# Kernel tuning notes

Measured on AMD Instinct MI355X. Metric: run time of the kernel, lower is better.

## Reference

```python
import jax, jax.numpy as jnp
import numpy as np

N = 10000      # nodes
E = 50000      # edges
NS = 48        # multiplicity of 0e (scalars)
NV = 10        # multiplicity of 1o (vectors)
NEF = 128      # n_edge_features
HID = 128      # hidden_features
W1N = NS * NS  # path 0e x 0e -> 0e
W2N = NS * NV  # path 0e x 1o -> 1o
W3N = NV * NV  # path 1o x 0e -> 1o
W4N = NV * NS  # path 1o x 1o -> 0e
WTOT = W1N + W2N + W3N + W4N  # tp.weight_numel = 3364
EPS = 1e-5
INV_SQRT3 = float(1.0 / np.sqrt(3.0))   # w3j(1,1,0) coefficient
NORM0 = float(1.0 / np.sqrt(NS + NV))   # path normalization into 0e output
NORM1 = float(1.0 / np.sqrt(NS + NV))   # path normalization into 1o output


def setup_inputs() -> dict:
    key = jax.random.key(0)
    ks = jax.random.split(key, 6)
    node_attr = jax.random.normal(ks[0], (N, NS + 3 * NV), jnp.float32)
    edge_index = jax.random.randint(ks[1], (2, E), 0, N, dtype=jnp.int32)
    edge_attr = jax.random.normal(ks[2], (E, NEF), jnp.float32)
    edge_sh = jax.random.normal(ks[3], (E, 4), jnp.float32)
    fc_w1 = jax.random.normal(ks[4], (NEF, HID), jnp.float32) / np.sqrt(NEF)
    fc_b1 = jnp.zeros((HID,), jnp.float32)
    fc_w2 = jax.random.normal(ks[5], (HID, WTOT), jnp.float32) / np.sqrt(HID)
    fc_b2 = jnp.zeros((WTOT,), jnp.float32)
    bn_weight = jnp.ones((NS + NV,), jnp.float32)  # affine scale per irrep
    bn_bias = jnp.zeros((NS,), jnp.float32)        # bias only for scalars
    return {"node_attr": node_attr, "edge_index": edge_index,
            "edge_attr": edge_attr, "edge_sh": edge_sh,
            "fc_w1": fc_w1, "fc_b1": fc_b1, "fc_w2": fc_w2, "fc_b2": fc_b2,
            "bn_weight": bn_weight, "bn_bias": bn_bias}


def reference(node_attr, edge_index, edge_attr, edge_sh,
              fc_w1, fc_b1, fc_w2, fc_b2, bn_weight, bn_bias):
    edge_src, edge_dst = edge_index[0], edge_index[1]

    # gather node features per edge
    x = node_attr[edge_dst]                       # [E, 78]
    s_in = x[:, :NS]                              # [E, NS] scalars (0e)
    v_in = x[:, NS:].reshape(E, NV, 3)            # [E, NV, 3] vectors (1o)
    sh0 = edge_sh[:, 0:1]                         # [E, 1]   sh 0e
    sh1 = edge_sh[:, 1:4]                         # [E, 3]   sh 1o

    # weight-generating MLP (per-edge tensor-product weights)
    h = jax.nn.relu(edge_attr @ fc_w1 + fc_b1)
    w = h @ fc_w2 + fc_b2                         # [E, 3364]
    w1 = w[:, :W1N].reshape(E, NS, NS)
    w2 = w[:, W1N:W1N + W2N].reshape(E, NS, NV)
    w3 = w[:, W1N + W2N:W1N + W2N + W3N].reshape(E, NV, NV)
    w4 = w[:, W1N + W2N + W3N:].reshape(E, NV, NS)

    # Clebsch-Gordan tensor product (4 paths)
    dot = jnp.einsum('evi,ei->ev', v_in, sh1) * INV_SQRT3      # 1o x 1o -> 0e
    out0 = (jnp.einsum('euv,eu->ev', w1, s_in) * sh0
            + jnp.einsum('euv,eu->ev', w4, dot)) * NORM0        # [E, NS]
    out1 = (jnp.einsum('euv,eu->ev', w2, s_in)[:, :, None] * sh1[:, None, :]
            + jnp.einsum('euv,eui->evi', w3, v_in) * sh0[:, :, None]) * NORM1  # [E, NV, 3]
    tp = jnp.concatenate([out0, out1.reshape(E, 3 * NV)], axis=-1)  # [E, 78]

    # scatter-mean to nodes
    summed = jax.ops.segment_sum(tp, edge_src, num_segments=N)
    cnt = jax.ops.segment_sum(jnp.ones((E,), tp.dtype), edge_src, num_segments=N)
    out = summed / jnp.maximum(cnt, 1.0)[:, None]

    # residual (in/out dims equal, so F.pad is a no-op)
    out = out + node_attr

    # e3nn-style equivariant BatchNorm (training mode, component normalization)
    s = out[:, :NS]
    v = out[:, NS:].reshape(N, NV, 3)
    s = s - s.mean(axis=0)
    s = s * jax.lax.rsqrt((s ** 2).mean(axis=0) + EPS) * bn_weight[:NS] + bn_bias
    vn = (v ** 2).mean(axis=-1).mean(axis=0)       # [NV] mean squared component
    v = v * (jax.lax.rsqrt(vn + EPS) * bn_weight[NS:])[None, :, None]
    return jnp.concatenate([s, v.reshape(N, 3 * NV)], axis=-1)
```

## Files before the change

### kernel.cpp

```cpp
#include <hip/hip_runtime.h>
#include <hip/hip_bf16.h>

#define NS 48
#define NV 10
#define NATT 78
#define HID 128
#define WTOT 3364
#define NEDGE 50000
#define NNODE 10000
#define EPAD 50048
#define EPSV 1e-5f
#define INV_SQRT3 0.57735026918962576f
#define NORM0 0.13130643285972254f
#define NORM1 0.13130643285972254f

#define FXS  2147483648.0f
#define FXSI (1.0 / 2147483648.0)
#define FXQ  268435456.0f
#define FXQI (1.0 / 268435456.0)

#define CPAD2 3744
#define NTILE 232
#define NGRP  78

#define NBLK_NODE 256

#define PREP_BLKS 1872
#define FC1_BLKS  782
#define ZERO_BYTES 6280000
#define ZERO_BLKS 1534

#define TP_BLKS 391

using half8 = __attribute__((ext_vector_type(8))) _Float16;
using f32x4 = __attribute__((ext_vector_type(4))) float;

__device__ __forceinline__ unsigned short f2h(float x) {
  union { _Float16 h; unsigned short u; } v;
  v.h = (_Float16)x;
  return v.u;
}

__device__ __forceinline__ void atomFx(unsigned long long* p, float x) {
  long long q = (long long)rintf(x * FXS);
  atomicAdd(p, (unsigned long long)q);
}

__device__ __forceinline__ int cp_to_src(int cp) {
  if (cp < 2304) return cp;
  if (cp < 2784) return 2884 + (cp - 2304);
  if (cp < 3552) { int t = cp - 2784; int u = t >> 4, v = t & 15;
                   return (v < 10) ? (2304 + u * 10 + v) : -1; }
  if (cp < 3712) { int t = cp - 3552; int u = t >> 4, v = t & 15;
                   return (v < 10) ? (2784 + u * 10 + v) : -1; }
  return -1;
}

__global__ __launch_bounds__(256) void k_front(const float* __restrict__ w2,
                                               unsigned short* __restrict__ Bt2,
                                               const float* __restrict__ ea,
                                               const float* __restrict__ w1,
                                               const float* __restrict__ b1,
                                               unsigned short* __restrict__ hbf,
                                               char* __restrict__ zbase) {
  __shared__ _Float16 w1T[128][136];
  const int bid = blockIdx.x;
  const int tid = threadIdx.x;

  if (bid < PREP_BLKS) {
    int idx = bid * 256 + tid;
    int cp = idx >> 7, k = idx & 127;
    int c_src = cp_to_src(cp);
    Bt2[idx] = (c_src >= 0) ? f2h(w2[(size_t)k * WTOT + c_src]) : (unsigned short)0;
    return;
  }
  if (bid >= PREP_BLKS + FC1_BLKS) {
    size_t off = ((size_t)(bid - PREP_BLKS - FC1_BLKS) * 256 + tid) * 16;
    if (off < ZERO_BYTES) *(uint4*)(zbase + off) = make_uint4(0, 0, 0, 0);
    return;
  }

  const int b  = bid - PREP_BLKS;
  const int e0 = b * 64;
  for (int i = tid; i < 128 * 128; i += 256) {
    int k = i >> 7, n = i & 127;
    w1T[n][k] = (_Float16)w1[i];
  }
  __syncthreads();

  const int lane = tid & 63, wid = tid >> 6;
  const int col = lane & 15, quad = lane >> 4;
  int e  = e0 + wid * 16 + col;
  int er = (e < NEDGE) ? e : 0;
  const float* ear = ea + (size_t)er * 128;
  half8 aF[4];
  #pragma unroll
  for (int ks = 0; ks < 4; ++ks) {
    float4 x0 = *(const float4*)&ear[ks * 32 + quad * 8];
    float4 x1 = *(const float4*)&ear[ks * 32 + quad * 8 + 4];
    half8 a;
    a[0] = (_Float16)x0.x; a[1] = (_Float16)x0.y; a[2] = (_Float16)x0.z; a[3] = (_Float16)x0.w;
    a[4] = (_Float16)x1.x; a[5] = (_Float16)x1.y; a[6] = (_Float16)x1.z; a[7] = (_Float16)x1.w;
    aF[ks] = a;
  }
  const int erow = e0 + wid * 16 + quad * 4;
  #pragma unroll
  for (int t = 0; t < 8; ++t) {
    float b1c = b1[t * 16 + col];
    f32x4 m = {0.f, 0.f, 0.f, 0.f};
    #pragma unroll
    for (int ks = 0; ks < 4; ++ks) {
      half8 bf = *(const half8*)&w1T[t * 16 + col][ks * 32 + quad * 8];
      m = __builtin_amdgcn_mfma_f32_16x16x32_f16(aF[ks], bf, m, 0, 0, 0);
    }
    #pragma unroll
    for (int r = 0; r < 4; ++r) {
      float h = fmaxf(m[r] + b1c, 0.f);
      hbf[(size_t)(erow + r) * 128 + t * 16 + col] = f2h(h);
    }
  }
}

__global__ __launch_bounds__(512, 4) void k_tp(const unsigned short* __restrict__ hbf,
                                               const unsigned short* __restrict__ Bt2,
                                               const float* __restrict__ fb2,
                                               const int* __restrict__ eidx,
                                               const float* __restrict__ node_attr,
                                               const float* __restrict__ esh,
                                               unsigned long long* __restrict__ summed,
                                               unsigned* __restrict__ cnt) {
  __shared__ half8    bufB[1536];
  __shared__ _Float16 sFT[48][128];
  __shared__ _Float16 vFL[128][30];
  __shared__ _Float16 b2pH[CPAD2];

  const int tid  = threadIdx.x;
  const int wid  = tid >> 6;
  const int lane = tid & 63;
  const int col  = lane & 15;
  const int quad = lane >> 4;
  const int e0   = blockIdx.x * 128;
  const int elb  = wid * 16 + quad * 4;

  float p0v[4];
  float sh1n[4][3];
  int   srcR[4];
  #pragma unroll
  for (int r = 0; r < 4; ++r) {
    int eg = e0 + elb + r;
    bool val = eg < NEDGE;
    srcR[r] = val ? eidx[eg] : -1;
    float sh0 = 0.f, x = 0.f, y = 0.f, z = 0.f;
    if (val) {
      float4 s4 = *(const float4*)&esh[(size_t)eg * 4];
      sh0 = s4.x; x = s4.y; y = s4.z; z = s4.w;
    }
    p0v[r] = sh0 * NORM0;
    sh1n[r][0] = x * NORM1; sh1n[r][1] = y * NORM1; sh1n[r][2] = z * NORM1;
  }
  for (int i = tid; i < CPAD2; i += 512) {
    int c_src = cp_to_src(i);
    b2pH[i] = (c_src >= 0) ? (_Float16)fb2[c_src] : (_Float16)0.f;
  }
  for (int i = tid; i < 128 * NATT; i += 512) {
    int el = i / NATT, a = i % NATT;
    int eg = e0 + el;
    int dst = (eg < NEDGE) ? eidx[NEDGE + eg] : -1;
    float x = (dst >= 0) ? node_attr[(size_t)dst * NATT + a] : 0.f;
    if (a < NS) sFT[a][el] = (_Float16)x; else vFL[el][a - NS] = (_Float16)x;
  }
  __syncthreads();

  half8 aF0, aF1, aF2, aF3;
  {
    const half8* hp = (const half8*)hbf;
    size_t arow = (size_t)(e0 + wid * 16 + col) * 16;
    aF0 = hp[arow + 0 * 4 + quad];
    aF1 = hp[arow + 1 * 4 + quad];
    aF2 = hp[arow + 2 * 4 + quad];
    aF3 = hp[arow + 3 * 4 + quad];
  }

  const char* bt2c = (const char*)Bt2;
  const int colS = (tid >> 4) & 15, k8sS = tid & 15;
  const size_t gOff = (size_t)(colS * 16 + (k8sS ^ colS)) * 16;

  #define STAGE3(G) do {                                                           \
    if (wid < 4) {                                                                 \
      int _t0 = (G) * 3;                                                           \
      char* _db = (char*)bufB + ((G) & 1) * 12288 + wid * 1024;                    \
      _Pragma("unroll")                                                            \
      for (int _t = 0; _t < 3; ++_t)                                               \
        __builtin_amdgcn_global_load_lds(                                          \
          (const __attribute__((address_space(1))) void*)(bt2c + (size_t)(_t0 + _t) * 4096 + gOff), \
          (__attribute__((address_space(3))) void*)(_db + _t * 4096), 16, 0, 0);   \
    }                                                                              \
  } while (0)

  STAGE3(0); STAGE3(1);

  float acc0[4][3] = {};
  float t1a[4] = {};
  float t3a[4][3] = {};

  const int k0 = (0 * 4 + quad) ^ col;
  const int k1 = (1 * 4 + quad) ^ col;
  const int k2 = (2 * 4 + quad) ^ col;
  const int k3 = (3 * 4 + quad) ^ col;
  const int cb = col * 16;

  #pragma unroll 1
  for (int p = 0; p < NGRP; ++p) {
    asm volatile("s_waitcnt vmcnt(0)\n\ts_barrier" ::: "memory");

    const int bb = ((p & 1) << 9) + ((p & 1) << 8) + cb;
    half8 b00 = bufB[bb +   0 + k0], b01 = bufB[bb +   0 + k1],
          b02 = bufB[bb +   0 + k2], b03 = bufB[bb +   0 + k3];
    half8 b10 = bufB[bb + 256 + k0], b11 = bufB[bb + 256 + k1],
          b12 = bufB[bb + 256 + k2], b13 = bufB[bb + 256 + k3];
    half8 b20 = bufB[bb + 512 + k0], b21 = bufB[bb + 512 + k1],
          b22 = bufB[bb + 512 + k2], b23 = bufB[bb + 512 + k3];

    __builtin_amdgcn_s_setprio(1);
    f32x4 m0 = {0.f, 0.f, 0.f, 0.f};
    f32x4 m1 = {0.f, 0.f, 0.f, 0.f};
    f32x4 m2 = {0.f, 0.f, 0.f, 0.f};
    m0 = __builtin_amdgcn_mfma_f32_16x16x32_f16(aF0, b00, m0, 0, 0, 0);
    m1 = __builtin_amdgcn_mfma_f32_16x16x32_f16(aF0, b10, m1, 0, 0, 0);
    m2 = __builtin_amdgcn_mfma_f32_16x16x32_f16(aF0, b20, m2, 0, 0, 0);
    m0 = __builtin_amdgcn_mfma_f32_16x16x32_f16(aF1, b01, m0, 0, 0, 0);
    m1 = __builtin_amdgcn_mfma_f32_16x16x32_f16(aF1, b11, m1, 0, 0, 0);
    m2 = __builtin_amdgcn_mfma_f32_16x16x32_f16(aF1, b21, m2, 0, 0, 0);
    m0 = __builtin_amdgcn_mfma_f32_16x16x32_f16(aF2, b02, m0, 0, 0, 0);
    m1 = __builtin_amdgcn_mfma_f32_16x16x32_f16(aF2, b12, m1, 0, 0, 0);
    m2 = __builtin_amdgcn_mfma_f32_16x16x32_f16(aF2, b22, m2, 0, 0, 0);
    m0 = __builtin_amdgcn_mfma_f32_16x16x32_f16(aF3, b03, m0, 0, 0, 0);
    m1 = __builtin_amdgcn_mfma_f32_16x16x32_f16(aF3, b13, m1, 0, 0, 0);
    m2 = __builtin_amdgcn_mfma_f32_16x16x32_f16(aF3, b23, m2, 0, 0, 0);
    __builtin_amdgcn_s_setprio(0);

    asm volatile("s_waitcnt lgkmcnt(0)\n\ts_barrier" ::: "memory");
    if (p < NGRP - 2) STAGE3(p + 2);

    float b2c0 = (float)b2pH[(p * 3 + 0) * 16 + col];
    float b2c1 = (float)b2pH[(p * 3 + 1) * 16 + col];
    float b2c2 = (float)b2pH[(p * 3 + 2) * 16 + col];
    if (p < 48) {
      #pragma unroll
      for (int r = 0; r < 4; ++r) {
        float sfac = (float)sFT[p][elb + r] * p0v[r];
        acc0[r][0] += (m0[r] + b2c0) * sfac;
        acc0[r][1] += (m1[r] + b2c1) * sfac;
        acc0[r][2] += (m2[r] + b2c2) * sfac;
      }
    } else if (p < 58) {
      int u3 = (p - 48) * 3;
      #pragma unroll
      for (int r = 0; r < 4; ++r) {
        int el = elb + r;
        float dfac = ((float)vFL[el][u3]     * sh1n[r][0] +
                      (float)vFL[el][u3 + 1] * sh1n[r][1] +
                      (float)vFL[el][u3 + 2] * sh1n[r][2]) * INV_SQRT3;
        acc0[r][0] += (m0[r] + b2c0) * dfac;
        acc0[r][1] += (m1[r] + b2c1) * dfac;
        acc0[r][2] += (m2[r] + b2c2) * dfac;
      }
    } else if (p < 74) {
      int u0 = (p - 58) * 3;
      #pragma unroll
      for (int r = 0; r < 4; ++r) {
        int el = elb + r;
        t1a[r] += (m0[r] + b2c0) * (float)sFT[u0][el]
                + (m1[r] + b2c1) * (float)sFT[u0 + 1][el]
                + (m2[r] + b2c2) * (float)sFT[u0 + 2][el];
      }
    } else {
      int ub = (p - 74) * 3;
      int T0 = p * 3;
      #pragma unroll
      for (int r = 0; r < 4; ++r) {
        int el = elb + r;
        {
          float w = m0[r] + b2c0;
          t3a[r][0] += w * (float)vFL[el][(ub + 0) * 3 + 0];
          t3a[r][1] += w * (float)vFL[el][(ub + 0) * 3 + 1];
          t3a[r][2] += w * (float)vFL[el][(ub + 0) * 3 + 2];
        }
        if (T0 + 1 < NTILE) {
          float w = m1[r] + b2c1;
          t3a[r][0] += w * (float)vFL[el][(ub + 1) * 3 + 0];
          t3a[r][1] += w * (float)vFL[el][(ub + 1) * 3 + 1];
          t3a[r][2] += w * (float)vFL[el][(ub + 1) * 3 + 2];
        }
        if (T0 + 2 < NTILE) {
          float w = m2[r] + b2c2;
          t3a[r][0] += w * (float)vFL[el][(ub + 2) * 3 + 0];
          t3a[r][1] += w * (float)vFL[el][(ub + 2) * 3 + 1];
          t3a[r][2] += w * (float)vFL[el][(ub + 2) * 3 + 2];
        }
      }
    }
  }
  #undef STAGE3

  #pragma unroll
  for (int r = 0; r < 4; ++r) {
    int src = srcR[r];
    if (src < 0) continue;
    unsigned long long* dp = &summed[(size_t)src * NATT];
    #pragma unroll
    for (int j = 0; j < 3; ++j)
      atomFx(dp + j * 16 + col, acc0[r][j]);
    if (col < 10) {
      float q0 = p0v[r];
      #pragma unroll
      for (int i = 0; i < 3; ++i)
        atomFx(dp + NS + col * 3 + i,
               t1a[r] * sh1n[r][i] + t3a[r][i] * q0);
    }
  }
  if (tid < 128) {
    int eg = e0 + tid;
    if (eg < NEDGE) atomicAdd(&cnt[eidx[eg]], 1u);
  }
}

__global__ __launch_bounds__(256) void k_node(const unsigned long long* __restrict__ summed,
                                              const unsigned* __restrict__ cnt,
                                              const float* __restrict__ node_attr,
                                              float* __restrict__ outp,
                                              unsigned long long* __restrict__ partials) {
  __shared__ unsigned long long ls[NS], lq[NS], lv[NV];
  int tid = threadIdx.x;
  if (tid < NS) { ls[tid] = 0ull; lq[tid] = 0ull; }
  if (tid < NV) lv[tid] = 0ull;
  __syncthreads();
  for (int i = blockIdx.x * 256 + tid; i < NNODE * NATT; i += NBLK_NODE * 256) {
    int row = i / NATT, colc = i % NATT;
    long long sv = (long long)summed[i];
    float sum = (float)((double)sv * FXSI);
    float x = sum / fmaxf((float)cnt[row], 1.f) + node_attr[i];
    outp[i] = x;
    if (colc < NS) {
      atomicAdd(&ls[colc], (unsigned long long)(long long)rintf(x * FXS));
      atomicAdd(&lq[colc], (unsigned long long)(long long)rintf(x * x * FXQ));
    } else {
      atomicAdd(&lv[(colc - NS) / 3], (unsigned long long)(long long)rintf(x * x * FXQ));
    }
  }
  __syncthreads();
  if (tid < 128) {
    unsigned long long v = 0ull;
    if (tid < NS)            v = ls[tid];
    else if (tid < 2 * NS)   v = lq[tid - NS];
    else if (tid < 96 + NV)  v = lv[tid - 96];
    partials[(size_t)blockIdx.x * 128 + tid] = v;
  }
}

__global__ __launch_bounds__(128) void k_stats(const unsigned long long* __restrict__ partials,
                                               unsigned long long* __restrict__ stats) {
  int c = threadIdx.x;
  unsigned long long s = 0ull;
  for (int b = 0; b < NBLK_NODE; ++b) s += partials[(size_t)b * 128 + c];
  stats[c] = s;
}

__global__ __launch_bounds__(256) void k_bn(const float* __restrict__ outp,
                                            const unsigned long long* __restrict__ stats,
                                            const float* __restrict__ bnw,
                                            const float* __restrict__ bnb,
                                            float* __restrict__ out) {
  int i = blockIdx.x * 256 + threadIdx.x;
  if (i >= NNODE * NATT) return;
  int colc = i % NATT;
  float x = outp[i];
  float r;
  if (colc < NS) {
    float mean = (float)((double)(long long)stats[colc] * (FXSI / NNODE));
    float ex2  = (float)((double)(long long)stats[NS + colc] * (FXQI / NNODE));
    float var  = ex2 - mean * mean;
    r = (x - mean) * rsqrtf(var + EPSV) * bnw[colc] + bnb[colc];
  } else {
    int u = (colc - NS) / 3;
    float vn = (float)((double)(long long)stats[96 + u] * (FXQI / (3.0 * NNODE)));
    r = x * rsqrtf(vn + EPSV) * bnw[NS + u];
  }
  out[i] = r;
}

extern "C" void kernel_launch(void* const* d_in, const int* in_sizes, int n_in,
                              void* d_out, int out_size, void* d_ws, size_t ws_size,
                              hipStream_t stream) {
  const float* node_attr = (const float*)d_in[0];
  const int*   eidx      = (const int*)d_in[1];
  const float* edge_attr = (const float*)d_in[2];
  const float* esh       = (const float*)d_in[3];
  const float* fw1       = (const float*)d_in[4];
  const float* fb1       = (const float*)d_in[5];
  const float* fw2       = (const float*)d_in[6];
  const float* fb2       = (const float*)d_in[7];
  const float* bnw       = (const float*)d_in[8];
  const float* bnb       = (const float*)d_in[9];
  float* out = (float*)d_out;

  char* ws = (char*)d_ws;
  unsigned short*     Bt2      = (unsigned short*)(ws + 0);
  unsigned short*     hbf      = (unsigned short*)(ws + 958464);
  unsigned long long* summed   = (unsigned long long*)(ws + 13770752);
  unsigned*           cnt      = (unsigned*)(ws + 20010752);
  float*              outp     = (float*)(ws + 0);
  unsigned long long* partials = (unsigned long long*)(ws + 3120000);
  unsigned long long* stats    = (unsigned long long*)(ws + 3382144);

  k_front<<<PREP_BLKS + FC1_BLKS + ZERO_BLKS, 256, 0, stream>>>(
      fw2, Bt2, edge_attr, fw1, fb1, hbf, ws + 13770752);
  k_tp<<<TP_BLKS, 512, 0, stream>>>(hbf, Bt2, fb2, eidx, node_attr, esh, summed, cnt);
  k_node<<<NBLK_NODE, 256, 0, stream>>>(summed, cnt, node_attr, outp, partials);
  k_stats<<<1, 128, 0, stream>>>(partials, stats);
  int nelem_blocks = (NNODE * NATT + 255) / 256;
  k_bn<<<nelem_blocks, 256, 0, stream>>>(outp, stats, bnw, bnb, out);
}
```

Baseline: 270.5 us.

## Halve TP block size, precompute padded bias in global, tile-transpose W2 prep

The tensor-product kernel now processes 64 edges per 256-thread block instead of 128 per 512, which doubles the block count to 782 and uses smaller LDS tiles. All four waves now stage the weight tiles themselves. The permuted fp16 fc2 bias is built once in the front kernel and read from global memory each iteration, rather than rebuilt per block in shared memory. Destination indices are cached in LDS, and the W2 transpose/permute prep goes through a coalesced shared-memory tile in 53 blocks instead of 1872 strided-read blocks. The trade-off is that each block streams the full weight matrix with fewer edges to reuse it, which doubles total weight traffic.

```diff
diff --git a/kernel.cpp b/kernel.cpp
--- a/kernel.cpp
+++ b/kernel.cpp
@@ -22,15 +22,18 @@
 #define CPAD2 3744
 #define NTILE 232
 #define NGRP  78
+#define B2G_BYTE_OFF 950272
 
 #define NBLK_NODE 256
 
-#define PREP_BLKS 1872
+#define PREPT_BLKS 53
 #define FC1_BLKS  782
 #define ZERO_BYTES 6280000
 #define ZERO_BLKS 1534
-
-#define TP_BLKS 391
+#define B2P_BLKS  15
+#define FC1_BASE  PREPT_BLKS
+#define ZERO_BASE (PREPT_BLKS + FC1_BLKS)
+#define B2P_BASE  (ZERO_BASE + ZERO_BLKS)
 
 using half8 = __attribute__((ext_vector_type(8))) _Float16;
 using f32x4 = __attribute__((ext_vector_type(4))) float;
@@ -62,29 +65,52 @@
                                                const float* __restrict__ w1,
                                                const float* __restrict__ b1,
                                                unsigned short* __restrict__ hbf,
+                                               const float* __restrict__ fb2,
                                                char* __restrict__ zbase) {
-  __shared__ _Float16 w1T[128][136];
+  __shared__ unsigned short w1T[128][136];
+  __shared__ unsigned short tileT[64][130];
   const int bid = blockIdx.x;
   const int tid = threadIdx.x;
 
-  if (bid < PREP_BLKS) {
-    int idx = bid * 256 + tid;
-    int cp = idx >> 7, k = idx & 127;
-    int c_src = cp_to_src(cp);
-    Bt2[idx] = (c_src >= 0) ? f2h(w2[(size_t)k * WTOT + c_src]) : (unsigned short)0;
+  if (bid < PREPT_BLKS) {
+    const int c0 = bid * 64;
+    for (int i = tid; i < 128 * 64; i += 256) {
+      int k = i >> 6, cl = i & 63, c = c0 + cl;
+      tileT[cl][k] = (c < WTOT) ? f2h(w2[(size_t)k * WTOT + c]) : (unsigned short)0;
+    }
+    __syncthreads();
+    for (int i = tid; i < 64 * 128; i += 256) {
+      int cl = i >> 7, k = i & 127, c = c0 + cl;
+      if (c >= WTOT) continue;
+      int cp;
+      if (c < 2304)      cp = c;
+      else if (c < 2784) { int t = c - 2304; cp = 2784 + (t / 10) * 16 + t % 10; }
+      else if (c < 2884) { int t = c - 2784; cp = 3552 + (t / 10) * 16 + t % 10; }
+      else               cp = 2304 + (c - 2884);
+      Bt2[(size_t)cp * 128 + k] = tileT[cl][k];
+    }
     return;
   }
-  if (bid >= PREP_BLKS + FC1_BLKS) {
-    size_t off = ((size_t)(bid - PREP_BLKS - FC1_BLKS) * 256 + tid) * 16;
+  if (bid >= B2P_BASE) {
+    int i = (bid - B2P_BASE) * 256 + tid;
+    if (i < 3712) {
+      int c_src = cp_to_src(i);
+      unsigned short* b2g = Bt2 + B2G_BYTE_OFF / 2;
+      b2g[i] = (c_src >= 0) ? f2h(fb2[c_src]) : f2h(0.f);
+    }
+    return;
+  }
+  if (bid >= ZERO_BASE) {
+    size_t off = ((size_t)(bid - ZERO_BASE) * 256 + tid) * 16;
     if (off < ZERO_BYTES) *(uint4*)(zbase + off) = make_uint4(0, 0, 0, 0);
     return;
   }
 
-  const int b  = bid - PREP_BLKS;
+  const int b  = bid - FC1_BASE;
   const int e0 = b * 64;
   for (int i = tid; i < 128 * 128; i += 256) {
     int k = i >> 7, n = i & 127;
-    w1T[n][k] = (_Float16)w1[i];
+    w1T[n][k] = f2h(w1[i]);
   }
   __syncthreads();
 
@@ -121,27 +147,32 @@
   }
 }
 
-__global__ __launch_bounds__(512, 4) void k_tp(const unsigned short* __restrict__ hbf,
+__global__ __launch_bounds__(256, 4) void k_tp(const unsigned short* __restrict__ hbf,
                                                const unsigned short* __restrict__ Bt2,
-                                               const float* __restrict__ fb2,
                                                const int* __restrict__ eidx,
                                                const float* __restrict__ node_attr,
                                                const float* __restrict__ esh,
                                                unsigned long long* __restrict__ summed,
                                                unsigned* __restrict__ cnt) {
   __shared__ half8    bufB[1536];
-  __shared__ _Float16 sFT[48][128];
-  __shared__ _Float16 vFL[128][30];
-  __shared__ _Float16 b2pH[CPAD2];
+  __shared__ _Float16 sFT[48][64];
+  __shared__ _Float16 vFL[64][30];
+  __shared__ int      dstL[64];
 
   const int tid  = threadIdx.x;
   const int wid  = tid >> 6;
   const int lane = tid & 63;
   const int col  = lane & 15;
   const int quad = lane >> 4;
-  const int e0   = blockIdx.x * 128;
+  const int e0   = blockIdx.x * 64;
   const int elb  = wid * 16 + quad * 4;
 
+  const _Float16* b2g = (const _Float16*)((const char*)Bt2 + B2G_BYTE_OFF);
+
+  if (tid < 64) {
+    int eg = e0 + tid;
+    dstL[tid] = (eg < NEDGE) ? eidx[NEDGE + eg] : -1;
+  }
   float p0v[4];
   float sh1n[4][3];
   int   srcR[4];
@@ -158,14 +189,10 @@
     p0v[r] = sh0 * NORM0;
     sh1n[r][0] = x * NORM1; sh1n[r][1] = y * NORM1; sh1n[r][2] = z * NORM1;
   }
-  for (int i = tid; i < CPAD2; i += 512) {
-    int c_src = cp_to_src(i);
-    b2pH[i] = (c_src >= 0) ? (_Float16)fb2[c_src] : (_Float16)0.f;
-  }
-  for (int i = tid; i < 128 * NATT; i += 512) {
+  __syncthreads();
+  for (int i = tid; i < 64 * NATT; i += 256) {
     int el = i / NATT, a = i % NATT;
-    int eg = e0 + el;
-    int dst = (eg < NEDGE) ? eidx[NEDGE + eg] : -1;
+    int dst = dstL[el];
     float x = (dst >= 0) ? node_attr[(size_t)dst * NATT + a] : 0.f;
     if (a < NS) sFT[a][el] = (_Float16)x; else vFL[el][a - NS] = (_Float16)x;
   }
@@ -182,19 +209,17 @@
   }
 
   const char* bt2c = (const char*)Bt2;
-  const int colS = (tid >> 4) & 15, k8sS = tid & 15;
+  const int colS = tid >> 4, k8sS = tid & 15;
   const size_t gOff = (size_t)(colS * 16 + (k8sS ^ colS)) * 16;
 
   #define STAGE3(G) do {                                                           \
-    if (wid < 4) {                                                                 \
-      int _t0 = (G) * 3;                                                           \
-      char* _db = (char*)bufB + ((G) & 1) * 12288 + wid * 1024;                    \
-      _Pragma("unroll")                                                            \
-      for (int _t = 0; _t < 3; ++_t)                                               \
-        __builtin_amdgcn_global_load_lds(                                          \
-          (const __attribute__((address_space(1))) void*)(bt2c + (size_t)(_t0 + _t) * 4096 + gOff), \
-          (__attribute__((address_space(3))) void*)(_db + _t * 4096), 16, 0, 0);   \
-    }                                                                              \
+    int _t0 = (G) * 3;                                                             \
+    char* _db = (char*)bufB + ((G) & 1) * 12288 + wid * 1024;                      \
+    _Pragma("unroll")                                                              \
+    for (int _t = 0; _t < 3; ++_t)                                                 \
+      __builtin_amdgcn_global_load_lds(                                            \
+        (const __attribute__((address_space(1))) void*)(bt2c + (size_t)(_t0 + _t) * 4096 + gOff), \
+        (__attribute__((address_space(3))) void*)(_db + _t * 4096), 16, 0, 0);     \
   } while (0)
 
   STAGE3(0); STAGE3(1);
@@ -212,6 +237,10 @@
   #pragma unroll 1
   for (int p = 0; p < NGRP; ++p) {
     asm volatile("s_waitcnt vmcnt(0)\n\ts_barrier" ::: "memory");
+
+    float b2c0 = (float)b2g[(p * 3 + 0) * 16 + col];
+    float b2c1 = (float)b2g[(p * 3 + 1) * 16 + col];
+    float b2c2 = (float)b2g[(p * 3 + 2) * 16 + col];
 
     const int bb = ((p & 1) << 9) + ((p & 1) << 8) + cb;
     half8 b00 = bufB[bb +   0 + k0], b01 = bufB[bb +   0 + k1],
@@ -242,9 +271,6 @@
     asm volatile("s_waitcnt lgkmcnt(0)\n\ts_barrier" ::: "memory");
     if (p < NGRP - 2) STAGE3(p + 2);
 
-    float b2c0 = (float)b2pH[(p * 3 + 0) * 16 + col];
-    float b2c1 = (float)b2pH[(p * 3 + 1) * 16 + col];
-    float b2c2 = (float)b2pH[(p * 3 + 2) * 16 + col];
     if (p < 48) {
       #pragma unroll
       for (int r = 0; r < 4; ++r) {
@@ -319,7 +345,7 @@
                t1a[r] * sh1n[r][i] + t3a[r][i] * q0);
     }
   }
-  if (tid < 128) {
+  if (tid < 64) {
     int eg = e0 + tid;
     if (eg < NEDGE) atomicAdd(&cnt[eidx[eg]], 1u);
   }
@@ -413,9 +439,9 @@
   unsigned long long* partials = (unsigned long long*)(ws + 3120000);
   unsigned long long* stats    = (unsigned long long*)(ws + 3382144);
 
-  k_front<<<PREP_BLKS + FC1_BLKS + ZERO_BLKS, 256, 0, stream>>>(
-      fw2, Bt2, edge_attr, fw1, fb1, hbf, ws + 13770752);
-  k_tp<<<TP_BLKS, 512, 0, stream>>>(hbf, Bt2, fb2, eidx, node_attr, esh, summed, cnt);
+  k_front<<<PREPT_BLKS + FC1_BLKS + ZERO_BLKS + B2P_BLKS, 256, 0, stream>>>(
+      fw2, Bt2, edge_attr, fw1, fb1, hbf, fb2, ws + 13770752);
+  k_tp<<<EPAD / 64, 256, 0, stream>>>(hbf, Bt2, eidx, node_attr, esh, summed, cnt);
   k_node<<<NBLK_NODE, 256, 0, stream>>>(summed, cnt, node_attr, outp, partials);
   k_stats<<<1, 128, 0, stream>>>(partials, stats);
   int nelem_blocks = (NNODE * NATT + 255) / 256;
```

New measurement: 273.2 us. No clear change (+1.0%).
